# Kernel tuning notes

Measured on AMD Instinct MI355X. Metric: run time of the kernel, lower is better.

The kernel has to match this reference:

```python
import jax, jax.numpy as jnp
import numpy as np

PATCH = (8, 8)          # (pw, ph) window_patch_shape
WINDOWS = (16, 16)      # (wy, wx) window grid
P = PATCH[0] * PATCH[1]


def _bias_indices():
    # relative position index pairs, exactly as in SwinSelfAttention class body
    pairs = np.array([[i, j] for i in range(PATCH[0]) for j in range(PATCH[1])])
    rel = pairs[:, None, :] - pairs[None, :, :] + PATCH[0] - 1  # [P,P,2]
    return rel[:, :, 0].astype(np.int32), rel[:, :, 1].astype(np.int32)


def _shift_mask():
    # generate_mask with apply_shift=True
    wy, wx = WINDOWS[1], WINDOWS[0]
    ph, pw = PATCH[1], PATCH[0]
    m = np.zeros((wy, wx, ph, pw, ph, pw), dtype=bool)
    sx, sy = pw // 2, ph // 2
    m[-1, :, :sy, :, sy:, :] = True
    m[-1, :, sy:, :, :sy, :] = True
    m[:, -1, :, :sx, :, sx:] = True
    m[:, -1, :, sx:, :, :sx] = True
    return m.reshape(wy, wx, P, P)


def setup_inputs() -> dict:
    key = jax.random.key(0)
    ks = jax.random.split(key, 10)
    B, E, H, D = 8, 512, 8, 64
    s = 1.0 / np.sqrt(E)
    iy, ix = _bias_indices()
    return {
        "patches": jax.random.normal(ks[0], (B, WINDOWS[1], WINDOWS[0], P, E), jnp.float32),
        "Wq": jax.random.normal(ks[1], (H, D, E), jnp.float32) * s,
        "bq": jax.random.normal(ks[2], (H, D), jnp.float32) * 0.02,
        "Wk": jax.random.normal(ks[3], (H, D, E), jnp.float32) * s,
        "bk": jax.random.normal(ks[4], (H, D), jnp.float32) * 0.02,
        "Wv": jax.random.normal(ks[5], (H, D, E), jnp.float32) * s,
        "bv": jax.random.normal(ks[6], (H, D), jnp.float32) * 0.02,
        "Wo": jax.random.normal(ks[7], (E, E), jnp.float32) * s,
        "bo": jax.random.normal(ks[8], (E,), jnp.float32) * 0.02,
        "pos_bias": jax.random.normal(ks[9], (2 * PATCH[1] - 1, 2 * PATCH[0] - 1), jnp.float32) * 0.02,
        "mask": jnp.asarray(_shift_mask()),
        "bias_idx_y": jnp.asarray(iy),
        "bias_idx_x": jnp.asarray(ix),
    }


def reference(patches, Wq, bq, Wk, bk, Wv, bv, Wo, bo, pos_bias, mask, bias_idx_y, bias_idx_x):
    # patches: [B, wy, wx, P, E]; W*: [H, D, E]; b*: [H, D]
    D = Wq.shape[1]
    q = jnp.einsum("byxpe,hde->byxhpd", patches, Wq) + bq[:, None, :]
    k = jnp.einsum("byxpe,hde->byxhpd", patches, Wk) + bk[:, None, :]
    v = jnp.einsum("byxpe,hde->byxhpd", patches, Wv) + bv[:, None, :]
    scores = jnp.einsum("byxhpd,byxhqd->byxhpq", q, k) / jnp.sqrt(jnp.asarray(D, patches.dtype))
    bias = pos_bias[bias_idx_y, bias_idx_x]                     # [P, P]
    scores = scores + bias
    scores = jnp.where(mask[None, :, :, None, :, :], -jnp.inf, scores)
    weights = jax.nn.softmax(scores, axis=-1)                   # dropout rate 0 -> identity
    rep = jnp.einsum("byxhpq,byxhqd->byxhpd", weights, v)
    B, wy, wx, H, Pn, Dn = rep.shape
    rep = jnp.transpose(rep, (0, 1, 2, 4, 3, 5)).reshape(B, wy, wx, Pn, H * Dn)
    return rep @ Wo.T + bo
```

## Files before the change

### kernel.cpp

```cpp
#include <hip/hip_runtime.h>
#include <hip/hip_bf16.h>

typedef __attribute__((ext_vector_type(8))) short bf16x8;
typedef __attribute__((ext_vector_type(16))) float f32x16;
typedef __attribute__((ext_vector_type(4))) unsigned int u32x4;

#define MFMA32(a, b, c) __builtin_amdgcn_mfma_f32_32x32x16_bf16((a), (b), (c), 0, 0, 0)

static __device__ __forceinline__ unsigned int pkbf(float lo, float hi) {
  unsigned int r;
  asm("v_cvt_pk_bf16_f32 %0, %1, %2" : "=v"(r) : "v"(lo), "v"(hi));
  return r;
}

static __device__ __forceinline__ bf16x8 u4_to_bf8(u32x4 u) {
  union { u32x4 u; bf16x8 b; } cv;
  cv.u = u;
  return cv.b;
}

static __device__ __forceinline__ f32x16 z16() {
  f32x16 z;
#pragma unroll
  for (int i = 0; i < 16; ++i) z[i] = 0.0f;
  return z;
}

static __device__ __forceinline__ void tile2frag(const f32x16 t, int hi,
                                                 bf16x8* f0, bf16x8* f1) {
  unsigned int a0 = pkbf(t[0], t[1]), a1 = pkbf(t[2], t[3]);
  unsigned int b0 = pkbf(t[4], t[5]), b1 = pkbf(t[6], t[7]);
  unsigned int c0 = pkbf(t[8], t[9]), c1 = pkbf(t[10], t[11]);
  unsigned int d0 = pkbf(t[12], t[13]), d1 = pkbf(t[14], t[15]);
  unsigned int sa0 = __shfl_xor((int)a0, 32), sa1 = __shfl_xor((int)a1, 32);
  unsigned int sb0 = __shfl_xor((int)b0, 32), sb1 = __shfl_xor((int)b1, 32);
  unsigned int sc0 = __shfl_xor((int)c0, 32), sc1 = __shfl_xor((int)c1, 32);
  unsigned int sd0 = __shfl_xor((int)d0, 32), sd1 = __shfl_xor((int)d1, 32);
  u32x4 fa, fb;
  fa[0] = hi ? sb0 : a0; fa[1] = hi ? sb1 : a1;
  fa[2] = hi ? b0 : sa0; fa[3] = hi ? b1 : sa1;
  fb[0] = hi ? sd0 : c0; fb[1] = hi ? sd1 : c1;
  fb[2] = hi ? d0 : sc0; fb[3] = hi ? d1 : sc1;
  *f0 = u4_to_bf8(fa);
  *f1 = u4_to_bf8(fb);
}

template <int XFIRST>
static __device__ __forceinline__ void gemm4(
    const unsigned short* __restrict__ wp,
    const unsigned short* xr0, const unsigned short* xr1, int sw, int hi,
    f32x16& c00, f32x16& c01, f32x16& c10, f32x16& c11) {
  bf16x8 wbuf[2][2][4];
#pragma unroll
  for (int j = 0; j < 4; ++j) {
    wbuf[0][0][j] = *reinterpret_cast<const bf16x8*>(wp + j * 512);
    wbuf[0][1][j] = *reinterpret_cast<const bf16x8*>(wp + 16384 + j * 512);
  }
#pragma unroll
  for (int kb = 0; kb < 8; ++kb) {
    const int cur = kb & 1, nxt = cur ^ 1;
    if (kb < 7) {
#pragma unroll
      for (int j = 0; j < 4; ++j) {
        wbuf[nxt][0][j] =
            *reinterpret_cast<const bf16x8*>(wp + (kb * 4 + 4 + j) * 512);
        wbuf[nxt][1][j] =
            *reinterpret_cast<const bf16x8*>(wp + 16384 + (kb * 4 + 4 + j) * 512);
      }
    }
    bf16x8 xb0[4], xb1[4];
#pragma unroll
    for (int j = 0; j < 4; ++j) {
      const int eo = 8 * hi + 16 * (kb * 4 + j);
      xb0[j] = *reinterpret_cast<const bf16x8*>(xr0 + (eo ^ sw));
      xb1[j] = *reinterpret_cast<const bf16x8*>(xr1 + (eo ^ sw));
    }
    __builtin_amdgcn_s_setprio(1);
#pragma unroll
    for (int j = 0; j < 4; ++j) {
      if (XFIRST) {
        c00 = MFMA32(xb0[j], wbuf[cur][0][j], c00);
        c01 = MFMA32(xb1[j], wbuf[cur][0][j], c01);
        c10 = MFMA32(xb0[j], wbuf[cur][1][j], c10);
        c11 = MFMA32(xb1[j], wbuf[cur][1][j], c11);
      } else {
        c00 = MFMA32(wbuf[cur][0][j], xb0[j], c00);
        c01 = MFMA32(wbuf[cur][0][j], xb1[j], c01);
        c10 = MFMA32(wbuf[cur][1][j], xb0[j], c10);
        c11 = MFMA32(wbuf[cur][1][j], xb1[j], c11);
      }
    }
    __builtin_amdgcn_s_setprio(0);
  }
}

static __device__ __forceinline__ float sm_tp(f32x16& t0, f32x16& t1,
                                              const float* BmRow, int swz, int hi) {
#pragma unroll
  for (int q2 = 0; q2 < 4; ++q2) {
    float4 b0 = *reinterpret_cast<const float4*>(BmRow + ((8 * q2 + 4 * hi) ^ swz));
    float4 b1 = *reinterpret_cast<const float4*>(BmRow + ((32 + 8 * q2 + 4 * hi) ^ swz));
    t0[4 * q2 + 0] = fmaf(t0[4 * q2 + 0], 0.125f, b0.x);
    t0[4 * q2 + 1] = fmaf(t0[4 * q2 + 1], 0.125f, b0.y);
    t0[4 * q2 + 2] = fmaf(t0[4 * q2 + 2], 0.125f, b0.z);
    t0[4 * q2 + 3] = fmaf(t0[4 * q2 + 3], 0.125f, b0.w);
    t1[4 * q2 + 0] = fmaf(t1[4 * q2 + 0], 0.125f, b1.x);
    t1[4 * q2 + 1] = fmaf(t1[4 * q2 + 1], 0.125f, b1.y);
    t1[4 * q2 + 2] = fmaf(t1[4 * q2 + 2], 0.125f, b1.z);
    t1[4 * q2 + 3] = fmaf(t1[4 * q2 + 3], 0.125f, b1.w);
  }
  float mx = t0[0];
#pragma unroll
  for (int r = 1; r < 16; ++r) mx = fmaxf(mx, t0[r]);
#pragma unroll
  for (int r = 0; r < 16; ++r) mx = fmaxf(mx, t1[r]);
  mx = fmaxf(mx, __shfl_xor(mx, 32));
  float sum = 0.f;
#pragma unroll
  for (int r = 0; r < 16; ++r) { t0[r] = __expf(t0[r] - mx); sum += t0[r]; }
#pragma unroll
  for (int r = 0; r < 16; ++r) { t1[r] = __expf(t1[r] - mx); sum += t1[r]; }
  sum += __shfl_xor(sum, 32);
  return 1.0f / sum;
}

__global__ __launch_bounds__(256) void prep_weights(
    const float* __restrict__ Wq, const float* __restrict__ Wk,
    const float* __restrict__ Wv, const float* __restrict__ Wo,
    unsigned short* __restrict__ dst) {
  int i = blockIdx.x * 256 + threadIdx.x;
  int blk = i >> 12;
  int c = i & 4095;
  int td = c >> 11;
  int ke = (c >> 6) & 31;
  int lane = c & 63;
  int hi = lane >> 5, l31 = lane & 31;
  int row = 32 * td + l31;
  int e = 16 * ke + 8 * hi;
  int seg = blk >> 3, sub = blk & 7;
  const float* base = (seg == 0) ? Wq : (seg == 1) ? Wk : (seg == 2) ? Wv : Wo;
  const float* src = base + (size_t)(sub * 64 + row) * 512 + e;
  float4 v0 = reinterpret_cast<const float4*>(src)[0];
  float4 v1 = reinterpret_cast<const float4*>(src)[1];
  u32x4 o;
  o[0] = pkbf(v0.x, v0.y); o[1] = pkbf(v0.z, v0.w);
  o[2] = pkbf(v1.x, v1.y); o[3] = pkbf(v1.z, v1.w);
  *reinterpret_cast<u32x4*>(dst + (size_t)blk * 32768 + c * 8) = o;
}

__global__ __launch_bounds__(256, 2) void swin_fused(
    const float* __restrict__ patches,
    const float* __restrict__ bq, const float* __restrict__ bk,
    const float* __restrict__ bv, const float* __restrict__ bo,
    const float* __restrict__ posb,
    const unsigned short* __restrict__ Wbf,
    float* __restrict__ out) {
  __shared__ unsigned short XsRs[64 * 512];
  __shared__ float Bm[64 * 64];

  const int tid = threadIdx.x;
  const int bid = blockIdx.x;
  const int wxi = bid & 15;
  const int wyi = (bid >> 4) & 15;
  const int w = tid >> 6;
  const int lane = tid & 63;
  const int l31 = lane & 31;
  const int hi = lane >> 5;

  const float* Xg = patches + (size_t)bid * 32768;
#pragma unroll
  for (int it = 0; it < 16; ++it) {
    int p = it * 4 + w;
    int e0 = lane << 3;
    const float4* gp = reinterpret_cast<const float4*>(Xg + p * 512 + e0);
    float4 v0 = gp[0], v1 = gp[1];
    u32x4 xv;
    xv[0] = pkbf(v0.x, v0.y); xv[1] = pkbf(v0.z, v0.w);
    xv[2] = pkbf(v1.x, v1.y); xv[3] = pkbf(v1.z, v1.w);
    *reinterpret_cast<u32x4*>(XsRs + p * 512 + (e0 ^ ((p & 31) << 3))) = xv;
  }
#pragma unroll
  for (int ii = 0; ii < 16; ++ii) {
    int i = ii * 256 + tid;
    int p = i >> 6, k = i & 63;
    int pr = p >> 3, pc = p & 7, kr = k >> 3, kc = k & 7;
    float b = posb[(pr - kr + 7) * 15 + (pc - kc + 7)];
    bool mk = ((wyi == 15) && ((pr < 4) != (kr < 4))) ||
              ((wxi == 15) && ((pc < 4) != (kc < 4)));
    Bm[p * 64 + (k ^ ((p & 15) << 2))] = mk ? -1e30f : b;
  }
  __syncthreads();

  const int sw = l31 << 3;
  const unsigned short* xr0 = XsRs + l31 * 512;
  const unsigned short* xr1 = XsRs + (l31 + 32) * 512;

  uint2 rst[2][2][2][4];
  const int bswz = (l31 & 15) << 2;
#pragma unroll
  for (int hh = 0; hh < 2; ++hh) {
    const int h = w + 4 * hh;
    bf16x8 kf[2][4], qf[2][4];
    {
      f32x16 c00 = z16(), c01 = z16(), c10 = z16(), c11 = z16();
      gemm4<0>(Wbf + (size_t)(8 + h) * 32768 + lane * 8, xr0, xr1, sw, hi,
               c00, c01, c10, c11);
      const float* bg = bk + h * 64;
#pragma unroll
      for (int q2 = 0; q2 < 4; ++q2) {
        float4 b0 = *reinterpret_cast<const float4*>(bg + 8 * q2 + 4 * hi);
        float4 b1 = *reinterpret_cast<const float4*>(bg + 32 + 8 * q2 + 4 * hi);
        c00[4 * q2 + 0] += b0.x; c00[4 * q2 + 1] += b0.y;
        c00[4 * q2 + 2] += b0.z; c00[4 * q2 + 3] += b0.w;
        c01[4 * q2 + 0] += b0.x; c01[4 * q2 + 1] += b0.y;
        c01[4 * q2 + 2] += b0.z; c01[4 * q2 + 3] += b0.w;
        c10[4 * q2 + 0] += b1.x; c10[4 * q2 + 1] += b1.y;
        c10[4 * q2 + 2] += b1.z; c10[4 * q2 + 3] += b1.w;
        c11[4 * q2 + 0] += b1.x; c11[4 * q2 + 1] += b1.y;
        c11[4 * q2 + 2] += b1.z; c11[4 * q2 + 3] += b1.w;
      }
      tile2frag(c00, hi, &kf[0][0], &kf[0][1]);
      tile2frag(c10, hi, &kf[0][2], &kf[0][3]);
      tile2frag(c01, hi, &kf[1][0], &kf[1][1]);
      tile2frag(c11, hi, &kf[1][2], &kf[1][3]);
    }
    {
      f32x16 c00 = z16(), c01 = z16(), c10 = z16(), c11 = z16();
      gemm4<0>(Wbf + (size_t)(0 + h) * 32768 + lane * 8, xr0, xr1, sw, hi,
               c00, c01, c10, c11);
      const float* bg = bq + h * 64;
#pragma unroll
      for (int q2 = 0; q2 < 4; ++q2) {
        float4 b0 = *reinterpret_cast<const float4*>(bg + 8 * q2 + 4 * hi);
        float4 b1 = *reinterpret_cast<const float4*>(bg + 32 + 8 * q2 + 4 * hi);
        c00[4 * q2 + 0] += b0.x; c00[4 * q2 + 1] += b0.y;
        c00[4 * q2 + 2] += b0.z; c00[4 * q2 + 3] += b0.w;
        c01[4 * q2 + 0] += b0.x; c01[4 * q2 + 1] += b0.y;
        c01[4 * q2 + 2] += b0.z; c01[4 * q2 + 3] += b0.w;
        c10[4 * q2 + 0] += b1.x; c10[4 * q2 + 1] += b1.y;
        c10[4 * q2 + 2] += b1.z; c10[4 * q2 + 3] += b1.w;
        c11[4 * q2 + 0] += b1.x; c11[4 * q2 + 1] += b1.y;
        c11[4 * q2 + 2] += b1.z; c11[4 * q2 + 3] += b1.w;
      }
      tile2frag(c00, hi, &qf[0][0], &qf[0][1]);
      tile2frag(c10, hi, &qf[0][2], &qf[0][3]);
      tile2frag(c01, hi, &qf[1][0], &qf[1][1]);
      tile2frag(c11, hi, &qf[1][2], &qf[1][3]);
    }

    f32x16 s00 = z16(), s01 = z16(), s10 = z16(), s11 = z16();
    __builtin_amdgcn_s_setprio(1);
#pragma unroll
    for (int kd = 0; kd < 4; ++kd) {
      s00 = MFMA32(kf[0][kd], qf[0][kd], s00);
      s01 = MFMA32(kf[0][kd], qf[1][kd], s01);
      s10 = MFMA32(kf[1][kd], qf[0][kd], s10);
      s11 = MFMA32(kf[1][kd], qf[1][kd], s11);
    }
    __builtin_amdgcn_s_setprio(0);
    float sinv0 = sm_tp(s00, s10, Bm + l31 * 64, bswz, hi);
    float sinv1 = sm_tp(s01, s11, Bm + (l31 + 32) * 64, bswz, hi);
    bf16x8 pf[2][4];
    tile2frag(s00, hi, &pf[0][0], &pf[0][1]);
    tile2frag(s10, hi, &pf[0][2], &pf[0][3]);
    tile2frag(s01, hi, &pf[1][0], &pf[1][1]);
    tile2frag(s11, hi, &pf[1][2], &pf[1][3]);

    bf16x8 vf[2][4];
    {
      f32x16 c00 = z16(), c01 = z16(), c10 = z16(), c11 = z16();
      gemm4<1>(Wbf + (size_t)(16 + h) * 32768 + lane * 8, xr0, xr1, sw, hi,
               c00, c01, c10, c11);
      float bv0 = bv[h * 64 + l31];
      float bv1 = bv[h * 64 + l31 + 32];
#pragma unroll
      for (int r = 0; r < 16; ++r) {
        c00[r] += bv0; c01[r] += bv0;
        c10[r] += bv1; c11[r] += bv1;
      }
      tile2frag(c00, hi, &vf[0][0], &vf[0][1]);
      tile2frag(c01, hi, &vf[0][2], &vf[0][3]);
      tile2frag(c10, hi, &vf[1][0], &vf[1][1]);
      tile2frag(c11, hi, &vf[1][2], &vf[1][3]);
    }

    f32x16 r00 = z16(), r01 = z16(), r10 = z16(), r11 = z16();
    __builtin_amdgcn_s_setprio(1);
#pragma unroll
    for (int ks = 0; ks < 4; ++ks) {
      r00 = MFMA32(vf[0][ks], pf[0][ks], r00); r01 = MFMA32(vf[0][ks], pf[1][ks], r01);
      r10 = MFMA32(vf[1][ks], pf[0][ks], r10); r11 = MFMA32(vf[1][ks], pf[1][ks], r11);
    }
    __builtin_amdgcn_s_setprio(0);
#pragma unroll
    for (int r = 0; r < 16; ++r) {
      r00[r] *= sinv0; r10[r] *= sinv0;
      r01[r] *= sinv1; r11[r] *= sinv1;
    }
#pragma unroll
    for (int tp = 0; tp < 2; ++tp) {
      const f32x16& t0 = tp ? r01 : r00;
      const f32x16& t1 = tp ? r11 : r10;
#pragma unroll
      for (int q2 = 0; q2 < 4; ++q2) {
        rst[hh][tp][0][q2].x = pkbf(t0[4 * q2 + 0], t0[4 * q2 + 1]);
        rst[hh][tp][0][q2].y = pkbf(t0[4 * q2 + 2], t0[4 * q2 + 3]);
        rst[hh][tp][1][q2].x = pkbf(t1[4 * q2 + 0], t1[4 * q2 + 1]);
        rst[hh][tp][1][q2].y = pkbf(t1[4 * q2 + 2], t1[4 * q2 + 3]);
      }
    }
  }

  __syncthreads();

#pragma unroll
  for (int hh = 0; hh < 2; ++hh) {
    const int h = w + 4 * hh;
#pragma unroll
    for (int tp = 0; tp < 2; ++tp) {
      int p = l31 + 32 * tp;
      unsigned short* row = XsRs + p * 512;
      int swp = l31 << 3;
#pragma unroll
      for (int td = 0; td < 2; ++td) {
#pragma unroll
        for (int q2 = 0; q2 < 4; ++q2) {
          int ce = h * 64 + 32 * td + 8 * q2 + 4 * hi;
          *reinterpret_cast<uint2*>(row + (ce ^ swp)) = rst[hh][tp][td][q2];
        }
      }
    }
  }
  __syncthreads();

  float* og = out + (size_t)bid * 32768;
#pragma unroll
  for (int pass = 0; pass < 2; ++pass) {
    f32x16 a00 = z16(), a01 = z16(), a10 = z16(), a11 = z16();
    gemm4<1>(Wbf + (size_t)(24 + 2 * w + pass) * 32768 + lane * 8, xr0, xr1, sw,
             hi, a00, a01, a10, a11);
#pragma unroll
    for (int j = 0; j < 2; ++j) {
      int col0 = 128 * w + 64 * pass + 32 * j + l31;
      float bov = bo[col0];
#pragma unroll
      for (int tp = 0; tp < 2; ++tp) {
        const f32x16& t = j ? (tp ? a11 : a10) : (tp ? a01 : a00);
#pragma unroll
        for (int r = 0; r < 16; ++r) {
          int p = (r & 3) + 8 * (r >> 2) + 4 * hi + 32 * tp;
          og[p * 512 + col0] = t[r] + bov;
        }
      }
    }
  }
}

extern "C" void kernel_launch(void* const* d_in, const int* in_sizes, int n_in,
                              void* d_out, int out_size, void* d_ws, size_t ws_size,
                              hipStream_t stream) {
  const float* patches = (const float*)d_in[0];
  const float* Wq = (const float*)d_in[1];
  const float* bq = (const float*)d_in[2];
  const float* Wk = (const float*)d_in[3];
  const float* bk = (const float*)d_in[4];
  const float* Wv = (const float*)d_in[5];
  const float* bv = (const float*)d_in[6];
  const float* Wo = (const float*)d_in[7];
  const float* bo = (const float*)d_in[8];
  const float* posb = (const float*)d_in[9];
  unsigned short* wbf = (unsigned short*)d_ws;
  hipLaunchKernelGGL(prep_weights, dim3(512), dim3(256), 0, stream, Wq, Wk, Wv, Wo, wbf);
  hipLaunchKernelGGL(swin_fused, dim3(2048), dim3(256), 0, stream,
                     patches, bq, bk, bv, bo, posb, wbf, (float*)d_out);
}
```

Before: 426.4 us.

## Stage attention output through global output buffer in MFMA fragment layout

Instead of holding per-head attention results in registers and writing them back into shared memory for the output projection, each wave writes its results as bf16 MFMA fragments into the block's own slice of the output buffer, then reads them back from global memory for the Wo GEMM. This removes the large register array and one shared-memory round trip plus a barrier, and drops the occupancy hint to one block per CU. The rows 32-63 half is computed and stored first, then a barrier guards overwriting the scratch region with the rows 0-31 results. It adds global traffic through L2 and relies on careful ordering to avoid clobbering scratch data still being read by other waves.

```diff
diff --git a/kernel.cpp b/kernel.cpp
--- a/kernel.cpp
+++ b/kernel.cpp
@@ -148,14 +148,14 @@
   *reinterpret_cast<u32x4*>(dst + (size_t)blk * 32768 + c * 8) = o;
 }
 
-__global__ __launch_bounds__(256, 2) void swin_fused(
+__global__ __launch_bounds__(256, 1) void swin_fused(
     const float* __restrict__ patches,
     const float* __restrict__ bq, const float* __restrict__ bk,
     const float* __restrict__ bv, const float* __restrict__ bo,
     const float* __restrict__ posb,
     const unsigned short* __restrict__ Wbf,
     float* __restrict__ out) {
-  __shared__ unsigned short XsRs[64 * 512];
+  __shared__ unsigned short Xs[64 * 512];
   __shared__ float Bm[64 * 64];
 
   const int tid = threadIdx.x;
@@ -177,7 +177,7 @@
     u32x4 xv;
     xv[0] = pkbf(v0.x, v0.y); xv[1] = pkbf(v0.z, v0.w);
     xv[2] = pkbf(v1.x, v1.y); xv[3] = pkbf(v1.z, v1.w);
-    *reinterpret_cast<u32x4*>(XsRs + p * 512 + (e0 ^ ((p & 31) << 3))) = xv;
+    *reinterpret_cast<u32x4*>(Xs + p * 512 + (e0 ^ ((p & 31) << 3))) = xv;
   }
 #pragma unroll
   for (int ii = 0; ii < 16; ++ii) {
@@ -191,12 +191,13 @@
   }
   __syncthreads();
 
+  unsigned short* Rws = reinterpret_cast<unsigned short*>(out) + (size_t)bid * 65536;
+
   const int sw = l31 << 3;
-  const unsigned short* xr0 = XsRs + l31 * 512;
-  const unsigned short* xr1 = XsRs + (l31 + 32) * 512;
-
-  uint2 rst[2][2][2][4];
+  const unsigned short* xr0 = Xs + l31 * 512;
+  const unsigned short* xr1 = Xs + (l31 + 32) * 512;
   const int bswz = (l31 & 15) << 2;
+
 #pragma unroll
   for (int hh = 0; hh < 2; ++hh) {
     const int h = w + 4 * hh;
@@ -297,62 +298,95 @@
       r00[r] *= sinv0; r10[r] *= sinv0;
       r01[r] *= sinv1; r11[r] *= sinv1;
     }
-#pragma unroll
-    for (int tp = 0; tp < 2; ++tp) {
-      const f32x16& t0 = tp ? r01 : r00;
-      const f32x16& t1 = tp ? r11 : r10;
-#pragma unroll
-      for (int q2 = 0; q2 < 4; ++q2) {
-        rst[hh][tp][0][q2].x = pkbf(t0[4 * q2 + 0], t0[4 * q2 + 1]);
-        rst[hh][tp][0][q2].y = pkbf(t0[4 * q2 + 2], t0[4 * q2 + 3]);
-        rst[hh][tp][1][q2].x = pkbf(t1[4 * q2 + 0], t1[4 * q2 + 1]);
-        rst[hh][tp][1][q2].y = pkbf(t1[4 * q2 + 2], t1[4 * q2 + 3]);
-      }
+    {
+      bf16x8 f0, f1;
+      unsigned short* rl = Rws + lane * 8;
+      tile2frag(r00, hi, &f0, &f1);
+      *reinterpret_cast<bf16x8*>(rl + (h * 4 + 0) * 512) = f0;
+      *reinterpret_cast<bf16x8*>(rl + (h * 4 + 1) * 512) = f1;
+      tile2frag(r01, hi, &f0, &f1);
+      *reinterpret_cast<bf16x8*>(rl + 16384 + (h * 4 + 0) * 512) = f0;
+      *reinterpret_cast<bf16x8*>(rl + 16384 + (h * 4 + 1) * 512) = f1;
+      tile2frag(r10, hi, &f0, &f1);
+      *reinterpret_cast<bf16x8*>(rl + (h * 4 + 2) * 512) = f0;
+      *reinterpret_cast<bf16x8*>(rl + (h * 4 + 3) * 512) = f1;
+      tile2frag(r11, hi, &f0, &f1);
+      *reinterpret_cast<bf16x8*>(rl + 16384 + (h * 4 + 2) * 512) = f0;
+      *reinterpret_cast<bf16x8*>(rl + 16384 + (h * 4 + 3) * 512) = f1;
     }
   }
 
   __syncthreads();
 
-#pragma unroll
-  for (int hh = 0; hh < 2; ++hh) {
-    const int h = w + 4 * hh;
-#pragma unroll
-    for (int tp = 0; tp < 2; ++tp) {
-      int p = l31 + 32 * tp;
-      unsigned short* row = XsRs + p * 512;
-      int swp = l31 << 3;
-#pragma unroll
-      for (int td = 0; td < 2; ++td) {
-#pragma unroll
-        for (int q2 = 0; q2 < 4; ++q2) {
-          int ce = h * 64 + 32 * td + 8 * q2 + 4 * hi;
-          *reinterpret_cast<uint2*>(row + (ce ^ swp)) = rst[hh][tp][td][q2];
-        }
-      }
-    }
-  }
-  __syncthreads();
-
   float* og = out + (size_t)bid * 32768;
-#pragma unroll
-  for (int pass = 0; pass < 2; ++pass) {
-    f32x16 a00 = z16(), a01 = z16(), a10 = z16(), a11 = z16();
-    gemm4<1>(Wbf + (size_t)(24 + 2 * w + pass) * 32768 + lane * 8, xr0, xr1, sw,
-             hi, a00, a01, a10, a11);
-#pragma unroll
-    for (int j = 0; j < 2; ++j) {
-      int col0 = 128 * w + 64 * pass + 32 * j + l31;
-      float bov = bo[col0];
-#pragma unroll
-      for (int tp = 0; tp < 2; ++tp) {
-        const f32x16& t = j ? (tp ? a11 : a10) : (tp ? a01 : a00);
+  {
+    f32x16 a[2][2];
+#pragma unroll
+    for (int p2 = 0; p2 < 2; ++p2)
+#pragma unroll
+      for (int j = 0; j < 2; ++j) a[p2][j] = z16();
+    const unsigned short* rl = Rws + 16384 + lane * 8;
+#pragma unroll
+    for (int pass = 0; pass < 2; ++pass) {
+      const unsigned short* wp =
+          Wbf + (size_t)(24 + 2 * w + pass) * 32768 + lane * 8;
+#pragma unroll 4
+      for (int kc = 0; kc < 32; ++kc) {
+        bf16x8 r1 = *reinterpret_cast<const bf16x8*>(rl + kc * 512);
+        bf16x8 wo0 = *reinterpret_cast<const bf16x8*>(wp + kc * 512);
+        bf16x8 wo1 = *reinterpret_cast<const bf16x8*>(wp + 16384 + kc * 512);
+        a[pass][0] = MFMA32(r1, wo0, a[pass][0]);
+        a[pass][1] = MFMA32(r1, wo1, a[pass][1]);
+      }
+    }
+#pragma unroll
+    for (int pass = 0; pass < 2; ++pass)
+#pragma unroll
+      for (int j = 0; j < 2; ++j) {
+        int col0 = 128 * w + 64 * pass + 32 * j + l31;
+        float bov = bo[col0];
+        const f32x16& t = a[pass][j];
 #pragma unroll
         for (int r = 0; r < 16; ++r) {
-          int p = (r & 3) + 8 * (r >> 2) + 4 * hi + 32 * tp;
+          int p = (r & 3) + 8 * (r >> 2) + 4 * hi + 32;
           og[p * 512 + col0] = t[r] + bov;
         }
       }
-    }
+  }
+  {
+    f32x16 a[2][2];
+#pragma unroll
+    for (int p2 = 0; p2 < 2; ++p2)
+#pragma unroll
+      for (int j = 0; j < 2; ++j) a[p2][j] = z16();
+    const unsigned short* rl = Rws + lane * 8;
+#pragma unroll
+    for (int pass = 0; pass < 2; ++pass) {
+      const unsigned short* wp =
+          Wbf + (size_t)(24 + 2 * w + pass) * 32768 + lane * 8;
+#pragma unroll 4
+      for (int kc = 0; kc < 32; ++kc) {
+        bf16x8 r0 = *reinterpret_cast<const bf16x8*>(rl + kc * 512);
+        bf16x8 wo0 = *reinterpret_cast<const bf16x8*>(wp + kc * 512);
+        bf16x8 wo1 = *reinterpret_cast<const bf16x8*>(wp + 16384 + kc * 512);
+        a[pass][0] = MFMA32(r0, wo0, a[pass][0]);
+        a[pass][1] = MFMA32(r0, wo1, a[pass][1]);
+      }
+    }
+    __syncthreads();
+#pragma unroll
+    for (int pass = 0; pass < 2; ++pass)
+#pragma unroll
+      for (int j = 0; j < 2; ++j) {
+        int col0 = 128 * w + 64 * pass + 32 * j + l31;
+        float bov = bo[col0];
+        const f32x16& t = a[pass][j];
+#pragma unroll
+        for (int r = 0; r < 16; ++r) {
+          int p = (r & 3) + 8 * (r >> 2) + 4 * hi;
+          og[p * 512 + col0] = t[r] + bov;
+        }
+      }
   }
 }
 
```

After: 511.4 us. 1.2x slower.
